# Optimization experiments

Measured on AMD Instinct MI355X. Metric: run time of the kernel, lower is better.

The kernel has to match this reference:

```python
import jax, jax.numpy as jnp
import numpy as np

KH = KW = 5  # receptive field


def _pair_w(a, b):
    # a, b: [...] in [0,1] -> soft one-hot over the 2-bit address (a = high bit): [..., 4]
    sa = jnp.stack([1.0 - a, a], axis=-1)
    sb = jnp.stack([1.0 - b, b], axis=-1)
    return (sa[..., :, None] * sb[..., None, :]).reshape(*a.shape, 4)


def _lut_nodes(g, lut):
    # g: [N, T, M, 6] node inputs in [0,1]; lut: [T, M, 64] raw LUT params.
    # DWN-style differentiable LUT: out = sum_a sigmoid(lut[a]) * prod_j (x_j if bit_j else 1-x_j)
    T, M = lut.shape[0], lut.shape[1]
    p = jax.nn.sigmoid(lut).reshape(T, M, 4, 4, 4)  # bits grouped pairwise, MSB-first
    Wa = _pair_w(g[..., 0], g[..., 1])  # [N,T,M,4]
    Wb = _pair_w(g[..., 2], g[..., 3])
    Wc = _pair_w(g[..., 4], g[..., 5])
    return jnp.einsum('tmpqr,ntmp,ntmq,ntmr->ntm', p, Wa, Wb, Wc)


def _lut_layer(h, idx, lut):
    # h: [N, T, P] previous-layer activations per tree; idx: [T, M, 6] in [0,P)
    T = idx.shape[0]
    g = h[:, jnp.arange(T)[:, None, None], idx]  # gather: [N, T, M, 6]
    return _lut_nodes(g, lut)


def setup_inputs() -> dict:
    key = jax.random.key(0)
    ks = jax.random.split(key, 7)
    x = jax.random.uniform(ks[0], (64, 1, 8, 8), dtype=jnp.float32)
    idx0 = jax.random.randint(ks[1], (128, 36, 6), 0, 25, dtype=jnp.int32)
    lut0 = jax.random.normal(ks[2], (128, 36, 64), dtype=jnp.float32)
    idx1 = jax.random.randint(ks[3], (128, 6, 6), 0, 36, dtype=jnp.int32)
    lut1 = jax.random.normal(ks[4], (128, 6, 64), dtype=jnp.float32)
    idx2 = jax.random.randint(ks[5], (128, 1, 6), 0, 6, dtype=jnp.int32)
    lut2 = jax.random.normal(ks[6], (128, 1, 64), dtype=jnp.float32)
    return dict(x=x, idx0=idx0, lut0=lut0, idx1=idx1, lut1=lut1, idx2=idx2, lut2=lut2)


def reference(x, idx0, lut0, idx1, lut1, idx2, lut2):
    B, C, H, W = x.shape
    oh, ow = H - KH + 1, W - KW + 1  # stride 1, padding 0 (as in nn.Unfold here)
    # im2col unfold, channel-major then (kh, kw) -- matches nn.Unfold ordering
    patches = jnp.stack(
        [x[:, c, i:i + oh, j:j + ow] for c in range(C) for i in range(KH) for j in range(KW)],
        axis=1,
    )  # [B, C*KH*KW, oh, ow]
    feat = patches.reshape(B, C * KH * KW, oh * ow).transpose(0, 2, 1).reshape(-1, C * KH * KW)  # [N, 25]
    # layer 0: gather from shared patch features into every tree
    g0 = feat[:, idx0]                      # [N, T, 36, 6]
    h0 = _lut_nodes(g0, lut0)               # [N, T, 36]
    h1 = _lut_layer(h0, idx1, lut1)         # [N, T, 6]
    h2 = _lut_layer(h1, idx2, lut2)         # [N, T, 1]
    T = lut0.shape[0]
    out = h2[..., 0].reshape(B, oh * ow, T).transpose(0, 2, 1).reshape(B, T, oh, ow)
    return out
```

## Files before the change

kernel.cpp:

```cpp
#include <hip/hip_runtime.h>
#include <hip/hip_fp16.h>

#define T_TREES 128
#define M0 36
#define M1 6
#define NNODES 43
#define XPAD 67

typedef float v2f __attribute__((ext_vector_type(2)));

__device__ __forceinline__ float sigmoidf(float v) {
    return 1.f / (1.f + __expf(-v));
}

__device__ __forceinline__ void pair_w(v2f a, v2f b, v2f w[4]) {
    v2f ab = a * b;
    w[3] = ab;
    w[2] = a - ab;
    w[1] = b - ab;
    w[0] = (1.f - a) - w[1];
}

__device__ __forceinline__ v2f lut_node_v2(const float* __restrict__ P,
                                           v2f a, v2f b, v2f c,
                                           v2f d, v2f e, v2f f) {
    v2f wa[4], wb[4], wc[4];
    pair_w(a, b, wa);
    pair_w(c, d, wb);
    pair_w(e, f, wc);
    v2f acc = {0.f, 0.f};
#pragma unroll
    for (int p = 0; p < 4; ++p) {
        v2f tp = {0.f, 0.f};
#pragma unroll
        for (int q = 0; q < 4; ++q) {
            const float* Pq = P + p * 16 + q * 4;
            v2f tq = Pq[0] * wc[0] + Pq[1] * wc[1] + Pq[2] * wc[2] + Pq[3] * wc[3];
            tp += tq * wb[q];
        }
        acc += tp * wa[p];
    }
    return acc;
}

__global__ __launch_bounds__(256, 2) void fused_kernel(
    const float* __restrict__ x,
    const int* __restrict__ idx0, const float* __restrict__ lut0,
    const int* __restrict__ idx1, const float* __restrict__ lut1,
    const int* __restrict__ idx2, const float* __restrict__ lut2,
    float* __restrict__ out) {
    __shared__ float xs[16 * XPAD];
    __shared__ __align__(16) float Ps[NNODES * 64];
    __shared__ __half2 h0s[M0 * 128];
    __shared__ __align__(8) float h1s[M1 * 256];

    const int tid = threadIdx.x;
    const int bx = blockIdx.x;
    const int t = bx & 127;
    const int q = bx >> 7;

    const float* __restrict__ xq = x + q * 1024;
    for (int i = tid; i < 1024; i += 256)
        xs[(i >> 6) * XPAD + (i & 63)] = xq[i];
    for (int i = tid; i < NNODES * 64; i += 256) {
        float v;
        if (i < M0 * 64)              v = lut0[t * (M0 * 64) + i];
        else if (i < (M0 + M1) * 64)  v = lut1[t * (M1 * 64) + (i - M0 * 64)];
        else                          v = lut2[t * 64 + (i - (M0 + M1) * 64)];
        Ps[i] = sigmoidf(v);
    }
    __syncthreads();

    const int w = tid >> 6, ln = tid & 63;

#pragma unroll 1
    for (int k = 0; k < 9; ++k) {
        const int m = w * 9 + k;
        float P[64];
#pragma unroll
        for (int i = 0; i < 16; ++i) {
            float4 v = reinterpret_cast<const float4*>(Ps + m * 64)[i];
            P[4 * i] = v.x; P[4 * i + 1] = v.y; P[4 * i + 2] = v.z; P[4 * i + 3] = v.w;
        }
        const int* id = idx0 + (t * M0 + m) * 6;
        int di[6];
#pragma unroll
        for (int j = 0; j < 6; ++j) {
            int kk = id[j];
            int ii = (kk * 13) >> 6;
            di[j] = kk - 5 * ii + ii * 8;
        }
#pragma unroll
        for (int u = 0; u < 2; ++u) {
            int p = u * 64 + ln;
            int b = p >> 3;
            int s = (p & 7) * 2;
            int xb = b * XPAD + (s >> 2) * 8 + (s & 3);
            v2f g[6];
#pragma unroll
            for (int j = 0; j < 6; ++j) {
                int a0 = xb + di[j];
                g[j].x = xs[a0];
                g[j].y = xs[a0 + 1];
            }
            v2f r = lut_node_v2(P, g[0], g[1], g[2], g[3], g[4], g[5]);
            h0s[m * 128 + p] = __floats2half2_rn(r.x, r.y);
        }
    }
    __syncthreads();

#pragma unroll 1
    for (int m1 = w; m1 < M1; m1 += 4) {
        float P[64];
#pragma unroll
        for (int i = 0; i < 16; ++i) {
            float4 v = reinterpret_cast<const float4*>(Ps + (M0 + m1) * 64)[i];
            P[4 * i] = v.x; P[4 * i + 1] = v.y; P[4 * i + 2] = v.z; P[4 * i + 3] = v.w;
        }
        const int* id = idx1 + (t * M1 + m1) * 6;
#pragma unroll
        for (int u = 0; u < 2; ++u) {
            int p = u * 64 + ln;
            v2f g[6];
#pragma unroll
            for (int j = 0; j < 6; ++j) {
                float2 f = __half22float2(h0s[id[j] * 128 + p]);
                g[j].x = f.x; g[j].y = f.y;
            }
            v2f r = lut_node_v2(P, g[0], g[1], g[2], g[3], g[4], g[5]);
            *reinterpret_cast<v2f*>(h1s + m1 * 256 + 2 * p) = r;
        }
    }
    __syncthreads();

    if (tid < 128) {
        float P[64];
#pragma unroll
        for (int i = 0; i < 16; ++i) {
            float4 v = reinterpret_cast<const float4*>(Ps + (M0 + M1) * 64)[i];
            P[4 * i] = v.x; P[4 * i + 1] = v.y; P[4 * i + 2] = v.z; P[4 * i + 3] = v.w;
        }
        const int* id = idx2 + t * 6;
        int rl = 2 * tid;
        v2f g[6];
#pragma unroll
        for (int j = 0; j < 6; ++j)
            g[j] = *reinterpret_cast<const v2f*>(h1s + id[j] * 256 + rl);
        v2f o = lut_node_v2(P, g[0], g[1], g[2], g[3], g[4], g[5]);
        int row = q * 256 + rl;
        int b = row >> 4, s = row & 15;
        *reinterpret_cast<v2f*>(out + b * (T_TREES * 16) + t * 16 + s) = o;
    }
}

extern "C" void kernel_launch(void* const* d_in, const int* in_sizes, int n_in,
                              void* d_out, int out_size, void* d_ws, size_t ws_size,
                              hipStream_t stream) {
    const float* x    = (const float*)d_in[0];
    const int*   idx0 = (const int*)  d_in[1];
    const float* lut0 = (const float*)d_in[2];
    const int*   idx1 = (const int*)  d_in[3];
    const float* lut1 = (const float*)d_in[4];
    const int*   idx2 = (const int*)  d_in[5];
    const float* lut2 = (const float*)d_in[6];
    float* out = (float*)d_out;

    fused_kernel<<<dim3(4 * T_TREES), 256, 0, stream>>>(
        x, idx0, lut0, idx1, lut1, idx2, lut2, out);
}
```

Measured before the change: 22.56 us.

## Precompute LUT sigmoids in a separate kernel and double block count

Adds a pre-pass kernel that applies the sigmoid to all LUT parameters once and writes them to workspace. The main kernel then reads those values straight from global memory instead of recomputing and staging them in shared memory per block. It also halves the rows per block (one pair per lane instead of two), launching twice as many blocks with a higher occupancy hint. The cost is an extra kernel launch, global reads of the sigmoid table from every block, and less work per block; a fallback keeps the old kernel when workspace is too small.

```diff
diff --git a/kernel.cpp b/kernel.cpp
--- a/kernel.cpp
+++ b/kernel.cpp
@@ -6,11 +6,31 @@
 #define M1 6
 #define NNODES 43
 #define XPAD 67
+#define SLUT_ELEMS (T_TREES * NNODES * 64)
 
 typedef float v2f __attribute__((ext_vector_type(2)));
 
 __device__ __forceinline__ float sigmoidf(float v) {
     return 1.f / (1.f + __expf(-v));
+}
+
+__global__ __launch_bounds__(256) void sig_kernel(
+    const float* __restrict__ lut0, const float* __restrict__ lut1,
+    const float* __restrict__ lut2, float* __restrict__ slut) {
+    int i4 = blockIdx.x * 256 + threadIdx.x;
+    int j4 = i4 & 15;
+    int tn = i4 >> 4;
+    int t = tn / NNODES;
+    int node = tn - t * NNODES;
+    const float4* src;
+    if (node < M0)            src = (const float4*)lut0 + (t * M0 + node) * 16 + j4;
+    else if (node < M0 + M1)  src = (const float4*)lut1 + (t * M1 + (node - M0)) * 16 + j4;
+    else                      src = (const float4*)lut2 + t * 16 + j4;
+    float4 v = *src;
+    float4 r;
+    r.x = sigmoidf(v.x); r.y = sigmoidf(v.y);
+    r.z = sigmoidf(v.z); r.w = sigmoidf(v.w);
+    reinterpret_cast<float4*>(slut)[i4] = r;
 }
 
 __device__ __forceinline__ void pair_w(v2f a, v2f b, v2f w[4]) {
@@ -43,7 +63,98 @@
     return acc;
 }
 
-__global__ __launch_bounds__(256, 2) void fused_kernel(
+__device__ __forceinline__ void hoist_P(const float* __restrict__ src, float P[64]) {
+#pragma unroll
+    for (int i = 0; i < 16; ++i) {
+        float4 v = reinterpret_cast<const float4*>(src)[i];
+        P[4 * i] = v.x; P[4 * i + 1] = v.y; P[4 * i + 2] = v.z; P[4 * i + 3] = v.w;
+    }
+}
+
+__global__ __launch_bounds__(256, 4) void fused_kernel(
+    const float* __restrict__ x,
+    const int* __restrict__ idx0, const int* __restrict__ idx1,
+    const int* __restrict__ idx2, const float* __restrict__ slut,
+    float* __restrict__ out) {
+    __shared__ float xs[8 * XPAD];
+    __shared__ __half2 h0s[M0 * 64];
+    __shared__ __align__(8) float h1s[M1 * 128];
+
+    const int tid = threadIdx.x;
+    const int bx = blockIdx.x;
+    const int t = bx & 127;
+    const int e = bx >> 7;
+
+    const float* __restrict__ xq = x + e * 512;
+    for (int i = tid; i < 512; i += 256)
+        xs[(i >> 6) * XPAD + (i & 63)] = xq[i];
+    __syncthreads();
+
+    const int w = __builtin_amdgcn_readfirstlane(tid >> 6);
+    const int ln = tid & 63;
+    const float* __restrict__ slt = slut + t * (NNODES * 64);
+
+#pragma unroll 1
+    for (int k = 0; k < 9; ++k) {
+        const int m = w * 9 + k;
+        float P[64];
+        hoist_P(slt + m * 64, P);
+        const int* id = idx0 + (t * M0 + m) * 6;
+        int di[6];
+#pragma unroll
+        for (int j = 0; j < 6; ++j) {
+            int kk = id[j];
+            int ii = (kk * 13) >> 6;
+            di[j] = kk - 5 * ii + ii * 8;
+        }
+        int b = ln >> 3;
+        int s = (ln & 7) * 2;
+        int xb = b * XPAD + (s >> 2) * 8 + (s & 3);
+        v2f g[6];
+#pragma unroll
+        for (int j = 0; j < 6; ++j) {
+            int a0 = xb + di[j];
+            g[j].x = xs[a0];
+            g[j].y = xs[a0 + 1];
+        }
+        v2f r = lut_node_v2(P, g[0], g[1], g[2], g[3], g[4], g[5]);
+        h0s[m * 64 + ln] = __floats2half2_rn(r.x, r.y);
+    }
+    __syncthreads();
+
+#pragma unroll 1
+    for (int m1 = w; m1 < M1; m1 += 4) {
+        float P[64];
+        hoist_P(slt + (M0 + m1) * 64, P);
+        const int* id = idx1 + (t * M1 + m1) * 6;
+        v2f g[6];
+#pragma unroll
+        for (int j = 0; j < 6; ++j) {
+            float2 f = __half22float2(h0s[id[j] * 64 + ln]);
+            g[j].x = f.x; g[j].y = f.y;
+        }
+        v2f r = lut_node_v2(P, g[0], g[1], g[2], g[3], g[4], g[5]);
+        *reinterpret_cast<v2f*>(h1s + m1 * 128 + 2 * ln) = r;
+    }
+    __syncthreads();
+
+    if (tid < 64) {
+        float P[64];
+        hoist_P(slt + (M0 + M1) * 64, P);
+        const int* id = idx2 + t * 6;
+        int rl = 2 * tid;
+        v2f g[6];
+#pragma unroll
+        for (int j = 0; j < 6; ++j)
+            g[j] = *reinterpret_cast<const v2f*>(h1s + id[j] * 128 + rl);
+        v2f o = lut_node_v2(P, g[0], g[1], g[2], g[3], g[4], g[5]);
+        int row = e * 128 + rl;
+        int b = row >> 4, s = row & 15;
+        *reinterpret_cast<v2f*>(out + b * (T_TREES * 16) + t * 16 + s) = o;
+    }
+}
+
+__global__ __launch_bounds__(256, 2) void fused_fb_kernel(
     const float* __restrict__ x,
     const int* __restrict__ idx0, const float* __restrict__ lut0,
     const int* __restrict__ idx1, const float* __restrict__ lut1,
@@ -72,16 +183,11 @@
     __syncthreads();
 
     const int w = tid >> 6, ln = tid & 63;
-
 #pragma unroll 1
     for (int k = 0; k < 9; ++k) {
         const int m = w * 9 + k;
         float P[64];
-#pragma unroll
-        for (int i = 0; i < 16; ++i) {
-            float4 v = reinterpret_cast<const float4*>(Ps + m * 64)[i];
-            P[4 * i] = v.x; P[4 * i + 1] = v.y; P[4 * i + 2] = v.z; P[4 * i + 3] = v.w;
-        }
+        hoist_P(Ps + m * 64, P);
         const int* id = idx0 + (t * M0 + m) * 6;
         int di[6];
 #pragma unroll
@@ -108,15 +214,10 @@
         }
     }
     __syncthreads();
-
 #pragma unroll 1
     for (int m1 = w; m1 < M1; m1 += 4) {
         float P[64];
-#pragma unroll
-        for (int i = 0; i < 16; ++i) {
-            float4 v = reinterpret_cast<const float4*>(Ps + (M0 + m1) * 64)[i];
-            P[4 * i] = v.x; P[4 * i + 1] = v.y; P[4 * i + 2] = v.z; P[4 * i + 3] = v.w;
-        }
+        hoist_P(Ps + (M0 + m1) * 64, P);
         const int* id = idx1 + (t * M1 + m1) * 6;
 #pragma unroll
         for (int u = 0; u < 2; ++u) {
@@ -132,14 +233,9 @@
         }
     }
     __syncthreads();
-
     if (tid < 128) {
         float P[64];
-#pragma unroll
-        for (int i = 0; i < 16; ++i) {
-            float4 v = reinterpret_cast<const float4*>(Ps + (M0 + M1) * 64)[i];
-            P[4 * i] = v.x; P[4 * i + 1] = v.y; P[4 * i + 2] = v.z; P[4 * i + 3] = v.w;
-        }
+        hoist_P(Ps + (M0 + M1) * 64, P);
         const int* id = idx2 + t * 6;
         int rl = 2 * tid;
         v2f g[6];
@@ -165,6 +261,13 @@
     const float* lut2 = (const float*)d_in[6];
     float* out = (float*)d_out;
 
-    fused_kernel<<<dim3(4 * T_TREES), 256, 0, stream>>>(
-        x, idx0, lut0, idx1, lut1, idx2, lut2, out);
-}
+    if (ws_size >= (size_t)SLUT_ELEMS * sizeof(float)) {
+        float* slut = (float*)d_ws;
+        sig_kernel<<<SLUT_ELEMS / 4 / 256, 256, 0, stream>>>(lut0, lut1, lut2, slut);
+        fused_kernel<<<dim3(8 * T_TREES), 256, 0, stream>>>(
+            x, idx0, idx1, idx2, slut, out);
+    } else {
+        fused_fb_kernel<<<dim3(4 * T_TREES), 256, 0, stream>>>(
+            x, idx0, lut0, idx1, lut1, idx2, lut2, out);
+    }
+}
```

After: 24.25 us. 1.07x slower.

## Halve grid with 512-thread blocks and store sigmoid LUTs as fp16 in LDS

Applied to the files above, without the earlier changes.

Each block now handles half the batch (512 positions) for one tree instead of a quarter, so the per-tree LUT sigmoid preprocessing is amortized over twice as many positions and the grid shrinks to 256 blocks. The sigmoided LUT parameters are kept in shared memory as half2 and widened to float on load, halving LDS footprint and load traffic. Warp index is made uniform via readfirstlane and layer-0 nodes are strided across 8 waves. The risks are reduced precision in the LUT probabilities, and fewer blocks than the 512 before, which may underfill the GPU. Layer 0 also becomes uneven, since 36 nodes split over 8 waves.

```diff
diff --git a/kernel.cpp b/kernel.cpp
--- a/kernel.cpp
+++ b/kernel.cpp
@@ -5,6 +5,7 @@
 #define M0 36
 #define M1 6
 #define NNODES 43
+#define TREE_SL (NNODES * 64)
 #define XPAD 67
 
 typedef float v2f __attribute__((ext_vector_type(2)));
@@ -43,45 +44,60 @@
     return acc;
 }
 
-__global__ __launch_bounds__(256, 2) void fused_kernel(
+__device__ __forceinline__ void hoist_P16(const __half2* __restrict__ src, float P[64]) {
+#pragma unroll
+    for (int i = 0; i < 8; ++i) {
+        float4 v = reinterpret_cast<const float4*>(src)[i];
+        float2 f0 = __half22float2(__builtin_bit_cast(__half2, v.x));
+        float2 f1 = __half22float2(__builtin_bit_cast(__half2, v.y));
+        float2 f2 = __half22float2(__builtin_bit_cast(__half2, v.z));
+        float2 f3 = __half22float2(__builtin_bit_cast(__half2, v.w));
+        P[8 * i + 0] = f0.x; P[8 * i + 1] = f0.y;
+        P[8 * i + 2] = f1.x; P[8 * i + 3] = f1.y;
+        P[8 * i + 4] = f2.x; P[8 * i + 5] = f2.y;
+        P[8 * i + 6] = f3.x; P[8 * i + 7] = f3.y;
+    }
+}
+
+__global__ __launch_bounds__(512) void fused_kernel(
     const float* __restrict__ x,
     const int* __restrict__ idx0, const float* __restrict__ lut0,
     const int* __restrict__ idx1, const float* __restrict__ lut1,
     const int* __restrict__ idx2, const float* __restrict__ lut2,
     float* __restrict__ out) {
-    __shared__ float xs[16 * XPAD];
-    __shared__ __align__(16) float Ps[NNODES * 64];
-    __shared__ __half2 h0s[M0 * 128];
-    __shared__ __align__(8) float h1s[M1 * 256];
+    __shared__ float xs[32 * XPAD];
+    __shared__ __align__(16) __half2 Psh[NNODES * 32];
+    __shared__ __half2 h0s[M0 * 256];
+    __shared__ __align__(8) float h1s[M1 * 512];
 
     const int tid = threadIdx.x;
     const int bx = blockIdx.x;
     const int t = bx & 127;
-    const int q = bx >> 7;
+    const int h = bx >> 7;
 
-    const float* __restrict__ xq = x + q * 1024;
-    for (int i = tid; i < 1024; i += 256)
+    const float* __restrict__ xq = x + h * 2048;
+    for (int i = tid; i < 2048; i += 512)
         xs[(i >> 6) * XPAD + (i & 63)] = xq[i];
-    for (int i = tid; i < NNODES * 64; i += 256) {
-        float v;
-        if (i < M0 * 64)              v = lut0[t * (M0 * 64) + i];
-        else if (i < (M0 + M1) * 64)  v = lut1[t * (M1 * 64) + (i - M0 * 64)];
-        else                          v = lut2[t * 64 + (i - (M0 + M1) * 64)];
-        Ps[i] = sigmoidf(v);
+    for (int i = tid; i < TREE_SL / 2; i += 512) {
+        int e = 2 * i;
+        float2 v;
+        if (e < M0 * 64)
+            v = *reinterpret_cast<const float2*>(lut0 + t * (M0 * 64) + e);
+        else if (e < (M0 + M1) * 64)
+            v = *reinterpret_cast<const float2*>(lut1 + t * (M1 * 64) + (e - M0 * 64));
+        else
+            v = *reinterpret_cast<const float2*>(lut2 + t * 64 + (e - (M0 + M1) * 64));
+        Psh[i] = __floats2half2_rn(sigmoidf(v.x), sigmoidf(v.y));
     }
     __syncthreads();
 
-    const int w = tid >> 6, ln = tid & 63;
+    const int w = __builtin_amdgcn_readfirstlane(tid >> 6);
+    const int ln = tid & 63;
 
 #pragma unroll 1
-    for (int k = 0; k < 9; ++k) {
-        const int m = w * 9 + k;
+    for (int m = w; m < M0; m += 8) {
         float P[64];
-#pragma unroll
-        for (int i = 0; i < 16; ++i) {
-            float4 v = reinterpret_cast<const float4*>(Ps + m * 64)[i];
-            P[4 * i] = v.x; P[4 * i + 1] = v.y; P[4 * i + 2] = v.z; P[4 * i + 3] = v.w;
-        }
+        hoist_P16(Psh + m * 32, P);
         const int* id = idx0 + (t * M0 + m) * 6;
         int di[6];
 #pragma unroll
@@ -91,7 +107,7 @@
             di[j] = kk - 5 * ii + ii * 8;
         }
 #pragma unroll
-        for (int u = 0; u < 2; ++u) {
+        for (int u = 0; u < 4; ++u) {
             int p = u * 64 + ln;
             int b = p >> 3;
             int s = (p & 7) * 2;
@@ -104,50 +120,42 @@
                 g[j].y = xs[a0 + 1];
             }
             v2f r = lut_node_v2(P, g[0], g[1], g[2], g[3], g[4], g[5]);
-            h0s[m * 128 + p] = __floats2half2_rn(r.x, r.y);
+            h0s[m * 256 + p] = __floats2half2_rn(r.x, r.y);
         }
     }
     __syncthreads();
 
 #pragma unroll 1
-    for (int m1 = w; m1 < M1; m1 += 4) {
+    for (int m1 = w; m1 < M1; m1 += 8) {
         float P[64];
-#pragma unroll
-        for (int i = 0; i < 16; ++i) {
-            float4 v = reinterpret_cast<const float4*>(Ps + (M0 + m1) * 64)[i];
-            P[4 * i] = v.x; P[4 * i + 1] = v.y; P[4 * i + 2] = v.z; P[4 * i + 3] = v.w;
-        }
+        hoist_P16(Psh + (M0 + m1) * 32, P);
         const int* id = idx1 + (t * M1 + m1) * 6;
 #pragma unroll
-        for (int u = 0; u < 2; ++u) {
+        for (int u = 0; u < 4; ++u) {
             int p = u * 64 + ln;
             v2f g[6];
 #pragma unroll
             for (int j = 0; j < 6; ++j) {
-                float2 f = __half22float2(h0s[id[j] * 128 + p]);
+                float2 f = __half22float2(h0s[id[j] * 256 + p]);
                 g[j].x = f.x; g[j].y = f.y;
             }
             v2f r = lut_node_v2(P, g[0], g[1], g[2], g[3], g[4], g[5]);
-            *reinterpret_cast<v2f*>(h1s + m1 * 256 + 2 * p) = r;
+            *reinterpret_cast<v2f*>(h1s + m1 * 512 + 2 * p) = r;
         }
     }
     __syncthreads();
 
-    if (tid < 128) {
+    if (tid < 256) {
         float P[64];
-#pragma unroll
-        for (int i = 0; i < 16; ++i) {
-            float4 v = reinterpret_cast<const float4*>(Ps + (M0 + M1) * 64)[i];
-            P[4 * i] = v.x; P[4 * i + 1] = v.y; P[4 * i + 2] = v.z; P[4 * i + 3] = v.w;
-        }
+        hoist_P16(Psh + (M0 + M1) * 32, P);
         const int* id = idx2 + t * 6;
         int rl = 2 * tid;
         v2f g[6];
 #pragma unroll
         for (int j = 0; j < 6; ++j)
-            g[j] = *reinterpret_cast<const v2f*>(h1s + id[j] * 256 + rl);
+            g[j] = *reinterpret_cast<const v2f*>(h1s + id[j] * 512 + rl);
         v2f o = lut_node_v2(P, g[0], g[1], g[2], g[3], g[4], g[5]);
-        int row = q * 256 + rl;
+        int row = h * 512 + rl;
         int b = row >> 4, s = row & 15;
         *reinterpret_cast<v2f*>(out + b * (T_TREES * 16) + t * 16 + s) = o;
     }
@@ -165,6 +173,6 @@
     const float* lut2 = (const float*)d_in[6];
     float* out = (float*)d_out;
 
-    fused_kernel<<<dim3(4 * T_TREES), 256, 0, stream>>>(
+    fused_kernel<<<dim3(2 * T_TREES), 512, 0, stream>>>(
         x, idx0, lut0, idx1, lut1, idx2, lut2, out);
 }
```

Result: faster. 20.11 us (median of 2 runs) (-10.9%).
